# Kernel tuning notes

Measured on AMD Instinct MI355X. Metric: run time of the kernel, lower is better.

## Reference

```python
import jax, jax.numpy as jnp
import numpy as np

NUM_EXPERTS = 8
D_MODEL = 2048
D_FF = 4096
TOP_K = 2
NUM_TOKENS = 4096


def setup_inputs() -> dict:
    key = jax.random.key(0)
    k1, k2, k3, k4, k5, k6 = jax.random.split(key, 6)
    hidden_states = jax.random.normal(k1, (NUM_TOKENS, D_MODEL), dtype=jnp.float32)
    top_k_index = jax.random.randint(k2, (NUM_TOKENS, TOP_K), 0, NUM_EXPERTS)
    raw = jax.random.uniform(k3, (NUM_TOKENS, TOP_K), dtype=jnp.float32)
    top_k_weights = raw / jnp.sum(raw, axis=-1, keepdims=True)  # normalized router weights
    scale = 0.02
    Wg = jax.random.normal(k4, (NUM_EXPERTS, D_MODEL, D_FF), dtype=jnp.float32) * scale
    Wu = jax.random.normal(k5, (NUM_EXPERTS, D_MODEL, D_FF), dtype=jnp.float32) * scale
    Wd = jax.random.normal(k6, (NUM_EXPERTS, D_FF, D_MODEL), dtype=jnp.float32) * scale
    return {
        "hidden_states": hidden_states,
        "top_k_index": top_k_index,
        "top_k_weights": top_k_weights,
        "Wg": Wg,
        "Wu": Wu,
        "Wd": Wd,
    }


def reference(hidden_states, top_k_index, top_k_weights, Wg, Wu, Wd):
    T, D = hidden_states.shape
    E = Wg.shape[0]
    # Combine weights: [T, E], summing duplicate expert hits exactly as the
    # original loop's repeated index_add_ would.
    combine = jnp.zeros((T, E), dtype=top_k_weights.dtype)
    combine = combine.at[jnp.arange(T)[:, None], top_k_index].add(top_k_weights)
    # Dense all-experts SwiGLU (same math per token/expert as the gather loop)
    gate = jnp.einsum("td,edf->tef", hidden_states, Wg)   # [T, E, F]
    up = jnp.einsum("td,edf->tef", hidden_states, Wu)     # [T, E, F]
    h = jax.nn.silu(gate) * up                              # [T, E, F]
    expert_out = jnp.einsum("tef,efd->ted", h, Wd)          # [T, E, D]
    # Weighted scatter-combine
    final = jnp.einsum("ted,te->td", expert_out, combine)   # [T, D]
    return final
```

## Files before the change

kernel.cpp:

```cpp
#include <hip/hip_runtime.h>
#include <hip/hip_bf16.h>

#define NTOK 4096
#define DM   2048
#define DF   4096
#define NEXP 8
#define NPAD 10240
#define NPTILE 40

typedef __attribute__((ext_vector_type(4))) float f32x4;
typedef __attribute__((ext_vector_type(8))) short s16x8;
typedef __attribute__((ext_vector_type(2))) int   i32x2;

__device__ __forceinline__ unsigned short f2bf(float f) {
  union { float f; unsigned u; } x; x.f = f;
  unsigned r = x.u + 0x7fffu + ((x.u >> 16) & 1u);
  return (unsigned short)(r >> 16);
}
__device__ __forceinline__ unsigned pack2(float lo, float hi) {
  __hip_bfloat162 h2 = __float22bfloat162_rn(make_float2(lo, hi));
  return *reinterpret_cast<unsigned*>(&h2);
}
__device__ __forceinline__ int swz(int row, int ks) {
  return row * 32 + ((ks ^ ((row >> 1) & 3)) << 3);
}
__device__ __forceinline__ void g2l16(const void* g, void* l) {
  __builtin_amdgcn_global_load_lds(
      (const __attribute__((address_space(1))) void*)g,
      (__attribute__((address_space(3))) void*)l, 16, 0, 0);
}

#define BARRIER() asm volatile("s_barrier" ::: "memory")
#define WAITV(n)  asm volatile("s_waitcnt vmcnt(" #n ")" ::: "memory")

__global__ void k_zero_out(float* out) {
  int gid = blockIdx.x * 256 + threadIdx.x;
  *(f32x4*)(out + (size_t)gid * 4) = f32x4{0.f, 0.f, 0.f, 0.f};
}

__global__ void k_init(int* tokrow, int* counts, int* cursor) {
  int i = blockIdx.x * 256 + threadIdx.x;
  if (i < NPAD) tokrow[i] = 0;
  if (i < NEXP) { counts[i] = 0; cursor[i] = 0; }
}

__global__ void k_count(const int* __restrict__ idx, int* counts) {
  int t = blockIdx.x * 256 + threadIdx.x;
  if (t >= NTOK) return;
  int e0 = idx[2 * t], e1 = idx[2 * t + 1];
  atomicAdd(&counts[e0], 1);
  if (e1 != e0) atomicAdd(&counts[e1], 1);
}

__global__ void k_scan(const int* __restrict__ counts, int* poff) {
  if (threadIdx.x == 0) {
    int s = 0;
    for (int e = 0; e < NEXP; e++) {
      poff[e] = s;
      s += ((counts[e] + 255) & ~255);
    }
  }
}

__global__ void k_fill(const int* __restrict__ idx, const float* __restrict__ wts,
                       const int* __restrict__ poff, int* cursor,
                       int* tokrow, float* wrow) {
  int t = blockIdx.x * 256 + threadIdx.x;
  if (t >= NTOK) return;
  int e0 = idx[2 * t], e1 = idx[2 * t + 1];
  float w0 = wts[2 * t], w1 = wts[2 * t + 1];
  if (e0 == e1) {
    int g = poff[e0] + atomicAdd(&cursor[e0], 1);
    tokrow[g] = t; wrow[g] = w0 + w1;
  } else {
    int g0 = poff[e0] + atomicAdd(&cursor[e0], 1);
    tokrow[g0] = t; wrow[g0] = w0;
    int g1 = poff[e1] + atomicAdd(&cursor[e1], 1);
    tokrow[g1] = t; wrow[g1] = w1;
  }
}

__global__ void k_convX(const float* __restrict__ X, const int* __restrict__ tokrow,
                        short* __restrict__ Xg) {
  const int kt = blockIdx.x, tile = blockIdx.y, tid = threadIdx.x;
  const int part = tid & 7;
  short* dst = Xg + (size_t)(tile * 64 + kt) * 8192;
  #pragma unroll
  for (int it = 0; it < 8; it++) {
    int row = it * 32 + (tid >> 3);
    int tok = tokrow[tile * 256 + row];
    f32x4 v = *(const f32x4*)(X + (size_t)tok * DM + kt * 32 + part * 4);
    i32x2 p;
    p[0] = (int)pack2(v[0], v[1]);
    p[1] = (int)pack2(v[2], v[3]);
    int idx = row * 32 + (((part >> 1) ^ ((row >> 1) & 3)) << 3) + (part & 1) * 4;
    *(i32x2*)&dst[idx] = p;
  }
}

__global__ void k_convW(const float* __restrict__ W, short* __restrict__ dst,
                        int N, int K) {
  const int nt = blockIdx.x, kt = blockIdx.y, e = blockIdx.z;
  const int t = threadIdx.x;
  const int kg = t >> 5, nb = t & 31;
  const float* src = W + (size_t)e * K * N + (size_t)(kt * 32 + kg * 4) * N
                     + nt * 128 + nb * 4;
  f32x4 b0 = *(const f32x4*)(src);
  f32x4 b1 = *(const f32x4*)(src + N);
  f32x4 b2 = *(const f32x4*)(src + 2 * (size_t)N);
  f32x4 b3 = *(const f32x4*)(src + 3 * (size_t)N);
  short* img = dst + ((size_t)(e * (N / 128) + nt) * (K / 32) + kt) * 4096;
  const int c0 = kg >> 1, klo = (kg & 1) * 4;
  #pragma unroll
  for (int j = 0; j < 4; j++) {
    int nl = nb * 4 + j;
    i32x2 v;
    v[0] = (int)pack2(b0[j], b1[j]);
    v[1] = (int)pack2(b2[j], b3[j]);
    *(i32x2*)&img[nl * 32 + ((c0 ^ ((nl >> 1) & 3)) << 3) + klo] = v;
  }
}

__global__ __launch_bounds__(512, 2) void gemm1_kernel(
    const short* __restrict__ Xg, const short* __restrict__ Wgt,
    const short* __restrict__ Wut, const int* __restrict__ counts,
    const int* __restrict__ poff, unsigned short* __restrict__ Hs) {
  const int e = blockIdx.z;
  const int cnt = counts[e];
  const int m0 = blockIdx.y * 256;
  if (m0 >= cnt) return;
  const int nt = blockIdx.x, n0 = nt * 128;
  const int tileIdx = (poff[e] >> 8) + blockIdx.y;

  __shared__ __attribute__((aligned(16))) short As[4][8192];
  __shared__ __attribute__((aligned(16))) short Bs[4][2][4096];

  const int tid = threadIdx.x, wave = tid >> 6, lane = tid & 63;
  const int wm = wave >> 1, wn = wave & 1;
  const int lr = lane & 15, ks = lane >> 4;

  const short* aSrc = Xg + (size_t)tileIdx * 64 * 8192 + wave * 1024 + lane * 8;
  const short* gSrc = Wgt + (size_t)(e * 32 + nt) * 64 * 4096 + wave * 512 + lane * 8;
  const short* uSrc = Wut + (size_t)(e * 32 + nt) * 64 * 4096 + wave * 512 + lane * 8;

  f32x4 accg[4][4], accu[4][4];
  #pragma unroll
  for (int i = 0; i < 4; i++)
    #pragma unroll
    for (int j = 0; j < 4; j++) {
      accg[i][j] = f32x4{0.f, 0.f, 0.f, 0.f};
      accu[i][j] = f32x4{0.f, 0.f, 0.f, 0.f};
    }

  auto stageA = [&](int s, int kt) {
    g2l16(aSrc + (size_t)kt * 8192,       &As[s][wave * 1024]);
    g2l16(aSrc + (size_t)kt * 8192 + 512, &As[s][wave * 1024 + 512]);
  };
  auto stageB = [&](int s, int kt) {
    g2l16(gSrc + (size_t)kt * 4096,       &Bs[s][0][wave * 512]);
    g2l16(uSrc + (size_t)kt * 4096,       &Bs[s][1][wave * 512]);
  };

  const int nK = DM / 32;
  stageA(0, 0); stageB(0, 0);
  stageA(1, 1); stageB(1, 1);
  stageA(2, 2); stageB(2, 2);
  asm volatile("s_waitcnt vmcnt(8) lgkmcnt(0)" ::: "memory");
  BARRIER();

  for (int kt = 0; kt < nK; ++kt) {
    const int s = kt & 3;
    s16x8 af[4], bg[4], bu[4];
    if (kt + 3 < nK) stageA((kt + 3) & 3, kt + 3);
    #pragma unroll
    for (int mi = 0; mi < 4; mi++)
      af[mi] = *(const s16x8*)&As[s][swz(wm * 64 + mi * 16 + lr, ks)];
    #pragma unroll
    for (int ni = 0; ni < 4; ni++)
      bg[ni] = *(const s16x8*)&Bs[s][0][swz(wn * 64 + ni * 16 + lr, ks)];
    BARRIER();
    __builtin_amdgcn_s_setprio(1);
    #pragma unroll
    for (int mi = 0; mi < 4; mi++)
      #pragma unroll
      for (int ni = 0; ni < 4; ni++)
        accg[mi][ni] = __builtin_amdgcn_mfma_f32_16x16x32_bf16(af[mi], bg[ni], accg[mi][ni], 0, 0, 0);
    __builtin_amdgcn_s_setprio(0);
    BARRIER();
    if (kt + 3 < nK) stageB((kt + 3) & 3, kt + 3);
    #pragma unroll
    for (int ni = 0; ni < 4; ni++)
      bu[ni] = *(const s16x8*)&Bs[s][1][swz(wn * 64 + ni * 16 + lr, ks)];
    BARRIER();
    __builtin_amdgcn_s_setprio(1);
    #pragma unroll
    for (int mi = 0; mi < 4; mi++)
      #pragma unroll
      for (int ni = 0; ni < 4; ni++)
        accu[mi][ni] = __builtin_amdgcn_mfma_f32_16x16x32_bf16(af[mi], bu[ni], accu[mi][ni], 0, 0, 0);
    __builtin_amdgcn_s_setprio(0);
    if (kt + 1 < nK) {
      if (kt + 3 < nK)      { WAITV(8); }
      else if (kt + 2 < nK) { WAITV(4); }
      else                  { WAITV(0); }
      BARRIER();
    }
  }

  const size_t tb = (size_t)tileIdx * 128 * 8192;
  #pragma unroll
  for (int mi = 0; mi < 4; mi++) {
    #pragma unroll
    for (int r = 0; r < 4; r++) {
      int row = wm * 64 + mi * 16 + ks * 4 + r;
      if (m0 + row < cnt) {
        #pragma unroll
        for (int ni = 0; ni < 4; ni++) {
          int col = n0 + wn * 64 + ni * 16 + lr;
          float g = accg[mi][ni][r], u = accu[mi][ni][r];
          float sv = g / (1.f + __expf(-g));
          int ktH = col >> 5, kl = col & 31;
          Hs[tb + (size_t)ktH * 8192 + row * 32 +
             (((kl >> 3) ^ ((row >> 1) & 3)) << 3) + (kl & 7)] = f2bf(sv * u);
        }
      }
    }
  }
}

__global__ __launch_bounds__(256, 4) void gemm2_kernel(
    const unsigned short* __restrict__ Hs, const short* __restrict__ Wdt,
    const int* __restrict__ counts, const int* __restrict__ poff,
    const int* __restrict__ tokrow, const float* __restrict__ wrow,
    float* __restrict__ out) {
  const int e = blockIdx.z;
  const int cnt = counts[e];
  const int m0 = blockIdx.y * 128;
  if (m0 >= cnt) return;
  const int nt = blockIdx.x, n0 = nt * 128;
  const int tileIdx = (poff[e] >> 8) + (m0 >> 8);
  const int half = (m0 >> 7) & 1;

  __shared__ __attribute__((aligned(16))) short As[2][4096];
  __shared__ __attribute__((aligned(16))) short Bs[2][4096];
  __shared__ float wl[128];
  __shared__ int   tl[128];

  const int tid = threadIdx.x, wave = tid >> 6, lane = tid & 63;
  const int wm = wave >> 1, wn = wave & 1;
  const int lr = lane & 15, ks = lane >> 4;

  if (tid < 128) {
    int rp = poff[e] + m0 + tid;
    wl[tid] = wrow[rp];
    tl[tid] = tokrow[rp];
  }

  const unsigned short* aSrc = Hs + (size_t)tileIdx * 128 * 8192 + half * 4096
                               + wave * 1024 + lane * 8;
  const short* bSrc = Wdt + (size_t)(e * 16 + nt) * 128 * 4096 + wave * 1024 + lane * 8;

  f32x4 acc[4][4];
  #pragma unroll
  for (int i = 0; i < 4; i++)
    #pragma unroll
    for (int j = 0; j < 4; j++) acc[i][j] = f32x4{0.f, 0.f, 0.f, 0.f};

  auto stage = [&](int b, int kt) {
    g2l16(aSrc + (size_t)kt * 8192,       &As[b][wave * 1024]);
    g2l16(aSrc + (size_t)kt * 8192 + 512, &As[b][wave * 1024 + 512]);
    g2l16(bSrc + (size_t)kt * 4096,       &Bs[b][wave * 1024]);
    g2l16(bSrc + (size_t)kt * 4096 + 512, &Bs[b][wave * 1024 + 512]);
  };

  stage(0, 0);
  __syncthreads();
  int buf = 0;
  const int nK = DF / 32;
  for (int kt = 0; kt < nK; ++kt) {
    if (kt + 1 < nK) stage(buf ^ 1, kt + 1);
    s16x8 af[4], bf_[4];
    #pragma unroll
    for (int mi = 0; mi < 4; mi++)
      af[mi] = *(const s16x8*)&As[buf][swz(wm * 64 + mi * 16 + lr, ks)];
    #pragma unroll
    for (int ni = 0; ni < 4; ni++)
      bf_[ni] = *(const s16x8*)&Bs[buf][swz(wn * 64 + ni * 16 + lr, ks)];
    __builtin_amdgcn_s_setprio(1);
    #pragma unroll
    for (int mi = 0; mi < 4; mi++)
      #pragma unroll
      for (int ni = 0; ni < 4; ni++)
        acc[mi][ni] = __builtin_amdgcn_mfma_f32_16x16x32_bf16(af[mi], bf_[ni], acc[mi][ni], 0, 0, 0);
    __builtin_amdgcn_s_setprio(0);
    __syncthreads();
    buf ^= 1;
  }

  #pragma unroll
  for (int mi = 0; mi < 4; mi++) {
    #pragma unroll
    for (int r = 0; r < 4; r++) {
      int row = wm * 64 + mi * 16 + ks * 4 + r;
      if (m0 + row < cnt) {
        float wgt = wl[row];
        float* obase = out + (size_t)tl[row] * DM + n0 + wn * 64 + lr;
        #pragma unroll
        for (int ni = 0; ni < 4; ni++)
          atomicAdd(obase + ni * 16, acc[mi][ni][r] * wgt);
      }
    }
  }
}

extern "C" void kernel_launch(void* const* d_in, const int* in_sizes, int n_in,
                              void* d_out, int out_size, void* d_ws, size_t ws_size,
                              hipStream_t stream) {
  (void)in_sizes; (void)n_in; (void)out_size; (void)ws_size;
  const float* X   = (const float*)d_in[0];
  const int*   idx = (const int*)d_in[1];
  const float* wts = (const float*)d_in[2];
  const float* Wg  = (const float*)d_in[3];
  const float* Wu  = (const float*)d_in[4];
  const float* Wd  = (const float*)d_in[5];
  float* out = (float*)d_out;

  uint8_t* w = (uint8_t*)d_ws;
  int*   counts = (int*)(w + 0);
  int*   cursor = (int*)(w + 64);
  int*   poff   = (int*)(w + 128);
  int*   tokrow = (int*)(w + 4096);
  float* wrow   = (float*)(w + 49152);
  short* Xg     = (short*)(w + (1ull << 20));
  unsigned short* Hs = (unsigned short*)(w + (48ull << 20));
  short* Wgt    = (short*)(w + (128ull << 20));
  short* Wut    = (short*)(w + (256ull << 20));
  short* Wdt    = (short*)(w + (384ull << 20));

  k_zero_out<<<NTOK * DM / 1024, 256, 0, stream>>>(out);
  k_init<<<NPTILE, 256, 0, stream>>>(tokrow, counts, cursor);
  k_count<<<16, 256, 0, stream>>>(idx, counts);
  k_scan<<<1, 64, 0, stream>>>(counts, poff);
  k_fill<<<16, 256, 0, stream>>>(idx, wts, poff, cursor, tokrow, wrow);
  k_convX<<<dim3(DM / 32, NPTILE), 256, 0, stream>>>(X, tokrow, Xg);
  k_convW<<<dim3(DF / 128, DM / 32, NEXP), 256, 0, stream>>>(Wg, Wgt, DF, DM);
  k_convW<<<dim3(DF / 128, DM / 32, NEXP), 256, 0, stream>>>(Wu, Wut, DF, DM);
  k_convW<<<dim3(DM / 128, DF / 32, NEXP), 256, 0, stream>>>(Wd, Wdt, DM, DF);
  gemm1_kernel<<<dim3(DF / 128, 16, NEXP), 512, 0, stream>>>(Xg, Wgt, Wut, counts, poff, Hs);
  gemm2_kernel<<<dim3(DM / 128, 32, NEXP), 256, 0, stream>>>(Hs, Wdt, counts, poff, tokrow, wrow, out);
}
```

Baseline: 1.005 ms.

## Widen gemm2 N-tile to 256 and merge gemm1 gate/up staging phases

gemm2 now computes two 128-wide N subtiles per block, so each A (H) tile loaded into shared memory is reused across 256 output columns. This halves the grid in N and the repeated A traffic, at the cost of double the accumulators, which is why launch bounds drop to 2 blocks per CU. gemm1 now stages A and both B tiles in one step, loads gate and up fragments together, and interleaves the two MFMA chains. This removes two of the three barriers per k-iteration but raises register pressure.

```diff
diff --git a/kernel.cpp b/kernel.cpp
--- a/kernel.cpp
+++ b/kernel.cpp
@@ -152,52 +152,38 @@
       accu[i][j] = f32x4{0.f, 0.f, 0.f, 0.f};
     }
 
-  auto stageA = [&](int s, int kt) {
+  auto stage = [&](int s, int kt) {
     g2l16(aSrc + (size_t)kt * 8192,       &As[s][wave * 1024]);
     g2l16(aSrc + (size_t)kt * 8192 + 512, &As[s][wave * 1024 + 512]);
-  };
-  auto stageB = [&](int s, int kt) {
     g2l16(gSrc + (size_t)kt * 4096,       &Bs[s][0][wave * 512]);
     g2l16(uSrc + (size_t)kt * 4096,       &Bs[s][1][wave * 512]);
   };
 
   const int nK = DM / 32;
-  stageA(0, 0); stageB(0, 0);
-  stageA(1, 1); stageB(1, 1);
-  stageA(2, 2); stageB(2, 2);
+  stage(0, 0); stage(1, 1); stage(2, 2);
   asm volatile("s_waitcnt vmcnt(8) lgkmcnt(0)" ::: "memory");
   BARRIER();
 
   for (int kt = 0; kt < nK; ++kt) {
     const int s = kt & 3;
+    if (kt + 3 < nK) stage((kt + 3) & 3, kt + 3);
     s16x8 af[4], bg[4], bu[4];
-    if (kt + 3 < nK) stageA((kt + 3) & 3, kt + 3);
     #pragma unroll
     for (int mi = 0; mi < 4; mi++)
       af[mi] = *(const s16x8*)&As[s][swz(wm * 64 + mi * 16 + lr, ks)];
     #pragma unroll
-    for (int ni = 0; ni < 4; ni++)
+    for (int ni = 0; ni < 4; ni++) {
       bg[ni] = *(const s16x8*)&Bs[s][0][swz(wn * 64 + ni * 16 + lr, ks)];
-    BARRIER();
+      bu[ni] = *(const s16x8*)&Bs[s][1][swz(wn * 64 + ni * 16 + lr, ks)];
+    }
     __builtin_amdgcn_s_setprio(1);
     #pragma unroll
     for (int mi = 0; mi < 4; mi++)
       #pragma unroll
-      for (int ni = 0; ni < 4; ni++)
+      for (int ni = 0; ni < 4; ni++) {
         accg[mi][ni] = __builtin_amdgcn_mfma_f32_16x16x32_bf16(af[mi], bg[ni], accg[mi][ni], 0, 0, 0);
-    __builtin_amdgcn_s_setprio(0);
-    BARRIER();
-    if (kt + 3 < nK) stageB((kt + 3) & 3, kt + 3);
-    #pragma unroll
-    for (int ni = 0; ni < 4; ni++)
-      bu[ni] = *(const s16x8*)&Bs[s][1][swz(wn * 64 + ni * 16 + lr, ks)];
-    BARRIER();
-    __builtin_amdgcn_s_setprio(1);
-    #pragma unroll
-    for (int mi = 0; mi < 4; mi++)
-      #pragma unroll
-      for (int ni = 0; ni < 4; ni++)
         accu[mi][ni] = __builtin_amdgcn_mfma_f32_16x16x32_bf16(af[mi], bu[ni], accu[mi][ni], 0, 0, 0);
+      }
     __builtin_amdgcn_s_setprio(0);
     if (kt + 1 < nK) {
       if (kt + 3 < nK)      { WAITV(8); }
@@ -228,7 +214,7 @@
   }
 }
 
-__global__ __launch_bounds__(256, 4) void gemm2_kernel(
+__global__ __launch_bounds__(256, 2) void gemm2_kernel(
     const unsigned short* __restrict__ Hs, const short* __restrict__ Wdt,
     const int* __restrict__ counts, const int* __restrict__ poff,
     const int* __restrict__ tokrow, const float* __restrict__ wrow,
@@ -237,12 +223,12 @@
   const int cnt = counts[e];
   const int m0 = blockIdx.y * 128;
   if (m0 >= cnt) return;
-  const int nt = blockIdx.x, n0 = nt * 128;
+  const int nt = blockIdx.x, n0 = nt * 256;
   const int tileIdx = (poff[e] >> 8) + (m0 >> 8);
   const int half = (m0 >> 7) & 1;
 
   __shared__ __attribute__((aligned(16))) short As[2][4096];
-  __shared__ __attribute__((aligned(16))) short Bs[2][4096];
+  __shared__ __attribute__((aligned(16))) short Bs[2][2][4096];
   __shared__ float wl[128];
   __shared__ int   tl[128];
 
@@ -258,19 +244,27 @@
 
   const unsigned short* aSrc = Hs + (size_t)tileIdx * 128 * 8192 + half * 4096
                                + wave * 1024 + lane * 8;
-  const short* bSrc = Wdt + (size_t)(e * 16 + nt) * 128 * 4096 + wave * 1024 + lane * 8;
-
-  f32x4 acc[4][4];
+  const short* b0Src = Wdt + (size_t)(e * 16 + 2 * nt) * 128 * 4096
+                       + wave * 1024 + lane * 8;
+  const short* b1Src = Wdt + (size_t)(e * 16 + 2 * nt + 1) * 128 * 4096
+                       + wave * 1024 + lane * 8;
+
+  f32x4 acc0[4][4], acc1[4][4];
   #pragma unroll
   for (int i = 0; i < 4; i++)
     #pragma unroll
-    for (int j = 0; j < 4; j++) acc[i][j] = f32x4{0.f, 0.f, 0.f, 0.f};
+    for (int j = 0; j < 4; j++) {
+      acc0[i][j] = f32x4{0.f, 0.f, 0.f, 0.f};
+      acc1[i][j] = f32x4{0.f, 0.f, 0.f, 0.f};
+    }
 
   auto stage = [&](int b, int kt) {
-    g2l16(aSrc + (size_t)kt * 8192,       &As[b][wave * 1024]);
-    g2l16(aSrc + (size_t)kt * 8192 + 512, &As[b][wave * 1024 + 512]);
-    g2l16(bSrc + (size_t)kt * 4096,       &Bs[b][wave * 1024]);
-    g2l16(bSrc + (size_t)kt * 4096 + 512, &Bs[b][wave * 1024 + 512]);
+    g2l16(aSrc + (size_t)kt * 8192,        &As[b][wave * 1024]);
+    g2l16(aSrc + (size_t)kt * 8192 + 512,  &As[b][wave * 1024 + 512]);
+    g2l16(b0Src + (size_t)kt * 4096,       &Bs[b][0][wave * 1024]);
+    g2l16(b0Src + (size_t)kt * 4096 + 512, &Bs[b][0][wave * 1024 + 512]);
+    g2l16(b1Src + (size_t)kt * 4096,       &Bs[b][1][wave * 1024]);
+    g2l16(b1Src + (size_t)kt * 4096 + 512, &Bs[b][1][wave * 1024 + 512]);
   };
 
   stage(0, 0);
@@ -279,19 +273,23 @@
   const int nK = DF / 32;
   for (int kt = 0; kt < nK; ++kt) {
     if (kt + 1 < nK) stage(buf ^ 1, kt + 1);
-    s16x8 af[4], bf_[4];
+    s16x8 af[4], b0f[4], b1f[4];
     #pragma unroll
     for (int mi = 0; mi < 4; mi++)
       af[mi] = *(const s16x8*)&As[buf][swz(wm * 64 + mi * 16 + lr, ks)];
     #pragma unroll
-    for (int ni = 0; ni < 4; ni++)
-      bf_[ni] = *(const s16x8*)&Bs[buf][swz(wn * 64 + ni * 16 + lr, ks)];
+    for (int ni = 0; ni < 4; ni++) {
+      b0f[ni] = *(const s16x8*)&Bs[buf][0][swz(wn * 64 + ni * 16 + lr, ks)];
+      b1f[ni] = *(const s16x8*)&Bs[buf][1][swz(wn * 64 + ni * 16 + lr, ks)];
+    }
     __builtin_amdgcn_s_setprio(1);
     #pragma unroll
     for (int mi = 0; mi < 4; mi++)
       #pragma unroll
-      for (int ni = 0; ni < 4; ni++)
-        acc[mi][ni] = __builtin_amdgcn_mfma_f32_16x16x32_bf16(af[mi], bf_[ni], acc[mi][ni], 0, 0, 0);
+      for (int ni = 0; ni < 4; ni++) {
+        acc0[mi][ni] = __builtin_amdgcn_mfma_f32_16x16x32_bf16(af[mi], b0f[ni], acc0[mi][ni], 0, 0, 0);
+        acc1[mi][ni] = __builtin_amdgcn_mfma_f32_16x16x32_bf16(af[mi], b1f[ni], acc1[mi][ni], 0, 0, 0);
+      }
     __builtin_amdgcn_s_setprio(0);
     __syncthreads();
     buf ^= 1;
@@ -301,13 +299,15 @@
   for (int mi = 0; mi < 4; mi++) {
     #pragma unroll
     for (int r = 0; r < 4; r++) {
-      int row = wm * 64 + mi * 16 + ks * 4 + r;
-      if (m0 + row < cnt) {
-        float wgt = wl[row];
-        float* obase = out + (size_t)tl[row] * DM + n0 + wn * 64 + lr;
+      int lrow = wm * 64 + mi * 16 + ks * 4 + r;
+      if (m0 + lrow < cnt) {
+        float wgt = wl[lrow];
+        float* obase = out + (size_t)tl[lrow] * DM + n0 + wn * 64 + lr;
         #pragma unroll
-        for (int ni = 0; ni < 4; ni++)
-          atomicAdd(obase + ni * 16, acc[mi][ni][r] * wgt);
+        for (int ni = 0; ni < 4; ni++) {
+          atomicAdd(obase + ni * 16,       acc0[mi][ni][r] * wgt);
+          atomicAdd(obase + 128 + ni * 16, acc1[mi][ni][r] * wgt);
+        }
       }
     }
   }
@@ -347,5 +347,5 @@
   k_convW<<<dim3(DF / 128, DM / 32, NEXP), 256, 0, stream>>>(Wu, Wut, DF, DM);
   k_convW<<<dim3(DM / 128, DF / 32, NEXP), 256, 0, stream>>>(Wd, Wdt, DM, DF);
   gemm1_kernel<<<dim3(DF / 128, 16, NEXP), 512, 0, stream>>>(Xg, Wgt, Wut, counts, poff, Hs);
-  gemm2_kernel<<<dim3(DM / 128, 32, NEXP), 256, 0, stream>>>(Hs, Wdt, counts, poff, tokrow, wrow, out);
-}
+  gemm2_kernel<<<dim3(DM / 256, 32, NEXP), 256, 0, stream>>>(Hs, Wdt, counts, poff, tokrow, wrow, out);
+}
```

New measurement: 887.0 us. 11.7% less time.
